# Kernel tuning notes

Hardware: AMD Instinct MI355X
Metric: run time of the kernel (lower is better)

## Reference

```python
import jax, jax.numpy as jnp
import numpy as np

N_RAYS, MAX_S, N_VOX, EMB, HID, L_VIEW = 8192, 64, 100000, 32, 128, 4


def view_pe(d):
    # NeRF positional encoding of view dirs: [N,3] -> [N, 3 + 6*L_VIEW]
    freqs = 2.0 ** jnp.arange(L_VIEW, dtype=d.dtype)
    ang = (d[..., None] * freqs).reshape(*d.shape[:-1], -1)  # [N, 3*L]
    return jnp.concatenate([d, jnp.sin(ang), jnp.cos(ang)], -1)


def setup_inputs() -> dict:
    key = jax.random.key(0)
    ks = jax.random.split(key, 16)
    rays_d = jax.random.normal(ks[0], (N_RAYS, 3), dtype=jnp.float32)
    rays_d = rays_d / jnp.linalg.norm(rays_d, axis=-1, keepdims=True)
    pts = jax.random.uniform(ks[1], (N_RAYS, MAX_S, 3), dtype=jnp.float32)
    t_vals = jnp.sort(jax.random.uniform(ks[2], (N_RAYS, MAX_S), dtype=jnp.float32) * 4.0, axis=-1)
    dists = jnp.concatenate([t_vals[:, 1:] - t_vals[:, :-1], jnp.full((N_RAYS, 1), 0.05, jnp.float32)], -1)
    # ragged per-ray sample counts -> -1 padded p2v_idx (as produced by the voxel point sampler)
    counts = jax.random.randint(ks[3], (N_RAYS,), 1, MAX_S + 1)
    ray_hits = jax.random.bernoulli(ks[4], 0.9, (N_RAYS,))
    valid = (jnp.arange(MAX_S)[None, :] < counts[:, None]) & ray_hits[:, None]
    idx = jax.random.randint(ks[5], (N_RAYS, MAX_S), 0, N_VOX)
    p2v_idx = jnp.where(valid, idx, -1).astype(jnp.int32)

    def lin(k, i, o):
        return jax.random.normal(k, (i, o), dtype=jnp.float32) * np.float32(1.0 / np.sqrt(i))

    return dict(
        rays_d=rays_d, pts=pts, t_vals=t_vals, dists=dists,
        p2v_idx=p2v_idx, ray_hits=ray_hits,
        vox_emb=jax.random.normal(ks[6], (N_VOX, EMB), dtype=jnp.float32) * 0.1,
        Wpts=lin(ks[7], 3, EMB),
        W1=lin(ks[8], EMB, HID), b1=jnp.zeros((HID,), jnp.float32),
        W2=lin(ks[9], HID, HID), b2=jnp.zeros((HID,), jnp.float32),
        Wsig=lin(ks[10], HID, 1), bsig=jnp.zeros((1,), jnp.float32),
        Wfeat=lin(ks[11], HID, HID), bfeat=jnp.zeros((HID,), jnp.float32),
        Wc1=lin(ks[12], HID + 3 + 6 * L_VIEW, 64), bc1=jnp.zeros((64,), jnp.float32),
        Wc2=lin(ks[13], 64, 3), bc2=jnp.zeros((3,), jnp.float32),
    )


def reference(rays_d, pts, t_vals, dists, vox_emb, Wpts, W1, b1, W2, b2,
              Wsig, bsig, Wfeat, bfeat, Wc1, bc1, Wc2, bc2, p2v_idx, ray_hits):
    mask = p2v_idx >= 0                                   # [N,S] valid samples (mask_pts)
    idx = jnp.where(mask, p2v_idx, 0)
    # voxel_embedder: per-point voxel embedding gather + positional lift
    ve = vox_emb[idx] + pts @ Wpts                        # [N,S,EMB]
    h = jax.nn.relu(ve @ W1 + b1)
    h = jax.nn.relu(h @ W2 + b2)                          # [N,S,HID]
    sigma = (h @ Wsig + bsig)[..., 0]                     # [N,S]
    feat = h @ Wfeat + bfeat                              # [N,S,HID]
    vemb = view_pe(rays_d)                                # [N,27]
    vemb = jnp.broadcast_to(vemb[:, None, :], (feat.shape[0], feat.shape[1], vemb.shape[-1]))
    c = jax.nn.relu(jnp.concatenate([feat, vemb], -1) @ Wc1 + bc1)
    rgb_raw = c @ Wc2 + bc2                               # [N,S,3]
    # masked_scatter semantics: invalid slots are 0 before the min_color remap
    rgb = (jnp.where(mask[..., None], rgb_raw, 0.0) + 1.0) * 0.5   # min_color = -1
    free_energy = jnp.where(mask, jax.nn.relu(sigma) * dists, 0.0)  # [N,S]
    # volumetric_rendering(with_dist=True)
    shifted = jnp.concatenate([jnp.zeros_like(free_energy[:, :1]), free_energy[:, :-1]], -1)
    T = jnp.exp(-jnp.cumsum(shifted, -1))
    weights = (1.0 - jnp.exp(-free_energy)) * T           # [N,S]
    comp_rgb = jnp.einsum('ns,nsc->nc', weights, rgb)     # [N,3]
    acc = weights.sum(-1)                                 # [N]
    depth = (weights * t_vals).sum(-1)
    disp = 1.0 / jnp.maximum(1e-10, depth / jnp.maximum(acc, 1e-10))
    # fill_in for missed rays (white_bkgd=False -> fill with 0)
    comp_rgb = jnp.where(ray_hits[:, None], comp_rgb, 0.0)
    disp = jnp.where(ray_hits, disp, 0.0)
    acc = jnp.where(ray_hits, acc, 0.0)
    return comp_rgb, disp, acc
```

## Files before the change

kernel.cpp:

```cpp
#include <hip/hip_runtime.h>
#include <stdint.h>


#define NRAYS 8192
#define MAXS  64
#define EMB   32
#define HID   128
#define NPE   27
#define CH    64
#define NPTS  (NRAYS * MAXS)
#define RCAP  16384

#define WS_WCOMB  0
#define WS_WPE    (WS_WCOMB + HID*CH)
#define WS_BCOMB  (WS_WPE + 32*CH)
#define WS_CCINIT (WS_BCOMB + CH)
#define WS_COUNTS (WS_CCINIT + NRAYS*CH)
#define WS_OFFS   (WS_COUNTS + NRAYS)
#define WS_TOTAL  (WS_OFFS + NRAYS)
#define WS_RCNT   (WS_TOTAL + 1)
#define WS_LIST   (WS_TOTAL + 4)
#define WS_PTOUT  (WS_LIST + NPTS)
#define WS_FRAGS  (WS_PTOUT + 4*NPTS)
#define WS_RLIST  (WS_FRAGS + 56*2*64*4)
#define WS_PTSC   (WS_RLIST + RCAP)

typedef __attribute__((ext_vector_type(8))) short bf16x8;
typedef __attribute__((ext_vector_type(4))) float f32x4;
union FI { int i[4]; int4 v; bf16x8 f; };

#define MFMA16(a, b, c) __builtin_amdgcn_mfma_f32_16x16x32_bf16(a, b, c, 0, 0, 0)

__device__ __forceinline__ f32x4 mfma3(bf16x8 ah, bf16x8 al, bf16x8 bh, bf16x8 bl,
                                       f32x4 c) {
  c = MFMA16(al, bh, c);
  c = MFMA16(ah, bl, c);
  c = MFMA16(ah, bh, c);
  return c;
}

__device__ __forceinline__ f32x4 mfma2(bf16x8 ah, bf16x8 bh, bf16x8 bl, f32x4 c) {
  c = MFMA16(ah, bl, c);
  c = MFMA16(ah, bh, c);
  return c;
}

__device__ __forceinline__ void split8(const float* x, bf16x8& hi, bf16x8& lo) {
  FI H, L;
#pragma unroll
  for (int r = 0; r < 4; ++r) {
    unsigned u0 = __float_as_uint(x[2 * r]);
    unsigned u1 = __float_as_uint(x[2 * r + 1]);
    unsigned h0 = u0 & 0xffff0000u, h1 = u1 & 0xffff0000u;
    unsigned l0 = __float_as_uint(x[2 * r] - __uint_as_float(h0));
    unsigned l1 = __float_as_uint(x[2 * r + 1] - __uint_as_float(h1));
    H.i[r] = (int)((h0 >> 16) | (h1 & 0xffff0000u));
    L.i[r] = (int)((l0 >> 16) | (l1 & 0xffff0000u));
  }
  hi = H.f; lo = L.f;
}

__device__ __forceinline__ unsigned short bf16rne(float v) {
  unsigned u = __float_as_uint(v);
  return (unsigned short)((u + 0x7fffu + ((u >> 16) & 1u)) >> 16);
}

__global__ __launch_bounds__(256) void prep_kernel(
    const float* __restrict__ Wfeat, const float* __restrict__ bfeat,
    const float* __restrict__ Wc1, const float* __restrict__ bc1,
    float* __restrict__ ws) {
  int idx = blockIdx.x * 256 + threadIdx.x;
  if (idx < HID * CH) {
    int m = idx >> 6, j = idx & 63;
    float s = 0.f;
    for (int f = 0; f < HID; ++f) s = fmaf(Wfeat[m * HID + f], Wc1[f * CH + j], s);
    ws[WS_WCOMB + idx] = s;
    return;
  }
  idx -= HID * CH;
  if (idx < 32 * CH) {
    int v = idx >> 6, j = idx & 63;
    ws[WS_WPE + idx] = (v < NPE) ? Wc1[(HID + v) * CH + j] : 0.f;
    return;
  }
  idx -= 32 * CH;
  if (idx < CH) {
    float s = bc1[idx];
    for (int f = 0; f < HID; ++f) s = fmaf(bfeat[f], Wc1[f * CH + idx], s);
    ws[WS_BCOMB + idx] = s;
    return;
  }
  idx -= CH;
  if (idx < 2) ((int*)(ws + WS_TOTAL))[idx] = 0;
}

__global__ __launch_bounds__(256) void prep2_kernel(
    const float* __restrict__ W1, const float* __restrict__ W2,
    float* __restrict__ ws) {
  int t = blockIdx.x * 256 + threadIdx.x;
  if (t >= 56 * 64) return;
  const int fid = t >> 6, lane = t & 63;
  const int n16 = lane & 15, quad = lane >> 4;
  float x[8];
  if (fid < 8) {
    const int n = fid * 16 + n16, k0 = quad * 8;
#pragma unroll
    for (int j = 0; j < 8; ++j) x[j] = W1[(k0 + j) * HID + n];
  } else if (fid < 40) {
    const int f = fid - 8, nt = f >> 2, s = f & 3;
    const int n = nt * 16 + n16, k0 = s * 32 + quad * 8;
#pragma unroll
    for (int j = 0; j < 8; ++j) x[j] = W2[(k0 + j) * HID + n];
  } else {
    const int f = fid - 40, nt = f >> 2, s = f & 3;
    const int n = nt * 16 + n16, k0 = s * 32 + quad * 8;
#pragma unroll
    for (int j = 0; j < 8; ++j) x[j] = ws[WS_WCOMB + (k0 + j) * CH + n];
  }
  FI H, L;
#pragma unroll
  for (int r = 0; r < 4; ++r) {
    unsigned u0 = __float_as_uint(x[2 * r]);
    unsigned u1 = __float_as_uint(x[2 * r + 1]);
    unsigned h0 = u0 & 0xffff0000u, h1 = u1 & 0xffff0000u;
    unsigned l0 = __float_as_uint(x[2 * r] - __uint_as_float(h0));
    unsigned l1 = __float_as_uint(x[2 * r + 1] - __uint_as_float(h1));
    H.i[r] = (int)((h0 >> 16) | (h1 & 0xffff0000u));
    L.i[r] = (int)((l0 >> 16) | (l1 & 0xffff0000u));
  }
  int4* o = (int4*)(ws + WS_FRAGS);
  o[(fid * 2 + 0) * 64 + lane] = H.v;
  o[(fid * 2 + 1) * 64 + lane] = L.v;
}

__global__ __launch_bounds__(256) void count_pe_kernel(
    const float* __restrict__ rays_d, const int* __restrict__ p2v,
    float* __restrict__ ws) {
  const int tid = threadIdx.x;
  const int ray = blockIdx.x * 4 + (tid >> 6);
  const int lane = tid & 63;
  const int v = p2v[ray * MAXS + lane];
  const unsigned long long ball = __ballot(v >= 0);
  if (lane == 0) ((int*)(ws + WS_COUNTS))[ray] = __popcll(ball);

  const float d0 = rays_d[ray * 3 + 0];
  const float d1 = rays_d[ray * 3 + 1];
  const float d2 = rays_d[ray * 3 + 2];
  float vemb[NPE];
  vemb[0] = d0; vemb[1] = d1; vemb[2] = d2;
#pragma unroll
  for (int i = 0; i < 3; ++i) {
    const float di = (i == 0) ? d0 : (i == 1) ? d1 : d2;
#pragma unroll
    for (int l = 0; l < 4; ++l) {
      const float ang = di * (float)(1 << l);
      vemb[3 + i * 4 + l] = __sinf(ang);
      vemb[3 + 12 + i * 4 + l] = __cosf(ang);
    }
  }
  float s = ws[WS_BCOMB + lane];
  const float* wpe = ws + WS_WPE;
#pragma unroll
  for (int vv = 0; vv < NPE; ++vv) s = fmaf(vemb[vv], wpe[vv * CH + lane], s);
  ws[WS_CCINIT + ray * CH + lane] = s;
}

__global__ __launch_bounds__(1024) void scan_kernel(float* __restrict__ ws) {
  const int* counts = (const int*)(ws + WS_COUNTS);
  int* offs = (int*)(ws + WS_OFFS);
  int* totalp = (int*)(ws + WS_TOTAL);
  __shared__ int wsum[16];
  const int tid = threadIdx.x;
  const int lane = tid & 63;
  const int base = tid * 8;
  if (tid == 0) ((int*)(ws + WS_RCNT))[0] = 0;
  int c[8], e[8];
  int run = 0;
#pragma unroll
  for (int i = 0; i < 8; ++i) { c[i] = counts[base + i]; e[i] = run; run += c[i]; }
  int inc = run;
#pragma unroll
  for (int off = 1; off < 64; off <<= 1) {
    int u = __shfl_up(inc, off, 64);
    if (lane >= off) inc += u;
  }
  const int wexcl = inc - run;
  if (lane == 63) wsum[tid >> 6] = inc;
  __syncthreads();
  if (tid < 16) {
    int v = wsum[tid];
    int inc2 = v;
#pragma unroll
    for (int off = 1; off < 16; off <<= 1) {
      int u = __shfl_up(inc2, off, 64);
      if (tid >= off) inc2 += u;
    }
    wsum[tid] = inc2 - v;
    if (tid == 15) totalp[0] = inc2;
  }
  __syncthreads();
  const int wbase = wsum[tid >> 6];
#pragma unroll
  for (int i = 0; i < 8; ++i) offs[base + i] = wbase + wexcl + e[i];
}

__global__ __launch_bounds__(256) void list_kernel(
    const int* __restrict__ p2v, const float* __restrict__ pts,
    float* __restrict__ ws) {
  const int tid = threadIdx.x;
  const int ray = blockIdx.x * 4 + (tid >> 6);
  const int lane = tid & 63;
  const int pidx = ray * MAXS + lane;
  const int gidx = p2v[pidx];
  const bool valid = gidx >= 0;
  const unsigned long long ball = __ballot(valid);
  const int rank = __popcll(ball & ((1ull << lane) - 1ull));
  if (valid) {
    const int off = ((const int*)(ws + WS_OFFS))[ray];
    const int slot = off + rank;
    ((int*)(ws + WS_LIST))[slot] = pidx;
    float4 pc;
    pc.x = pts[pidx * 3 + 0];
    pc.y = pts[pidx * 3 + 1];
    pc.z = pts[pidx * 3 + 2];
    pc.w = __int_as_float(gidx);
    ((float4*)(ws + WS_PTSC))[slot] = pc;
  }
}

__device__ __forceinline__ void ve_frag(const float* __restrict__ vox_emb,
                                        const float* __restrict__ Wpts,
                                        float4 pc, int quad,
                                        bf16x8& hi, bf16x8& lo) {
  float x[8];
  const int gidx = __float_as_int(pc.w);
  const float4* vr = (const float4*)vox_emb + gidx * 8 + quad * 2;
  const float4 va = vr[0], vb = vr[1];
  const float px = pc.x, py = pc.y, pz = pc.z;
  const float4* wp = (const float4*)Wpts;
  const float4 wa0 = wp[quad * 2 + 0], wa1 = wp[quad * 2 + 1];
  const float4 wb0 = wp[8 + quad * 2 + 0], wb1 = wp[8 + quad * 2 + 1];
  const float4 wc0 = wp[16 + quad * 2 + 0], wc1 = wp[16 + quad * 2 + 1];
  x[0] = va.x + fmaf(px, wa0.x, fmaf(py, wb0.x, pz * wc0.x));
  x[1] = va.y + fmaf(px, wa0.y, fmaf(py, wb0.y, pz * wc0.y));
  x[2] = va.z + fmaf(px, wa0.z, fmaf(py, wb0.z, pz * wc0.z));
  x[3] = va.w + fmaf(px, wa0.w, fmaf(py, wb0.w, pz * wc0.w));
  x[4] = vb.x + fmaf(px, wa1.x, fmaf(py, wb1.x, pz * wc1.x));
  x[5] = vb.y + fmaf(px, wa1.y, fmaf(py, wb1.y, pz * wc1.y));
  x[6] = vb.z + fmaf(px, wa1.z, fmaf(py, wb1.z, pz * wc1.z));
  x[7] = vb.w + fmaf(px, wa1.w, fmaf(py, wb1.w, pz * wc1.w));
  split8(x, hi, lo);
}

#define SROW 136

__global__ __launch_bounds__(128, 2) void mlp_mfma(
    const float* __restrict__ vox_emb, const float* __restrict__ Wpts,
    const float* __restrict__ b1, const float* __restrict__ b2,
    const float* __restrict__ Wsig, const float* __restrict__ bsig,
    const float* __restrict__ Wc2, const float* __restrict__ bc2,
    float* __restrict__ ws) {
  __shared__ __align__(16) unsigned short alds[32 * SROW];
  const int tid = threadIdx.x;
  const int wave = tid >> 6, lane = tid & 63;
  const int n16 = lane & 15, quad = lane >> 4;
  const int total = ((const int*)(ws + WS_TOTAL))[0];
  const int base = blockIdx.x * 32 + wave * 16;
  if (base >= total) return;
  const int* list = (const int*)(ws + WS_LIST);
  const int slot0 = min(base + n16, total - 1);
  const int pidx0 = list[slot0];
  const float4 pc0 = ((const float4*)(ws + WS_PTSC))[slot0];
  const int4* fb = (const int4*)(ws + WS_FRAGS);

  int4 B1f[16];
#pragma unroll
  for (int i = 0; i < 16; ++i) B1f[i] = fb[i * 64 + lane];

  bf16x8 a0h, a0l;
  ve_frag(vox_emb, Wpts, pc0, quad, a0h, a0l);

  int4 BL[16];
#pragma unroll
  for (int nt = 0; nt < 8; ++nt) {
    BL[2 * nt]     = fb[((8 + nt * 4) * 2 + 0) * 64 + lane];
    BL[2 * nt + 1] = fb[((8 + nt * 4) * 2 + 1) * 64 + lane];
  }

  f32x4 h[8];
#pragma unroll
  for (int nt = 0; nt < 8; ++nt) {
    const float bb = b1[nt * 16 + n16];
    h[nt] = (f32x4){bb, bb, bb, bb};
  }
#pragma unroll
  for (int nt = 0; nt < 8; ++nt) {
    FI H, L; H.v = B1f[2 * nt]; L.v = B1f[2 * nt + 1];
    h[nt] = mfma3(a0h, a0l, H.f, L.f, h[nt]);
  }
#pragma unroll
  for (int nt = 0; nt < 8; ++nt)
#pragma unroll
    for (int r = 0; r < 4; ++r) {
      const float v = fmaxf(h[nt][r], 0.f);
      const int row = wave * 16 + quad * 4 + r;
      const int gk = ((2 * nt + (n16 >> 3)) ^ (row & 7)) << 3;
      alds[row * SROW + gk + (n16 & 7)] = bf16rne(v);
    }

  f32x4 g[8];
#pragma unroll
  for (int nt = 0; nt < 8; ++nt) {
    const float bb = b2[nt * 16 + n16];
    g[nt] = (f32x4){bb, bb, bb, bb};
  }
  const int rrow0 = (wave * 16 + n16) * SROW;
  const int t7 = n16 & 7;
#pragma unroll
  for (int s = 0; s < 4; ++s) {
    const int gq = ((4 * s + quad) ^ t7) << 3;
    const bf16x8 A0h = *(const bf16x8*)&alds[rrow0 + gq];
#pragma unroll
    for (int nt = 0; nt < 8; ++nt) {
      FI H, L; H.v = BL[2 * nt]; L.v = BL[2 * nt + 1];
      g[nt] = mfma2(A0h, H.f, L.f, g[nt]);
    }
    if (s < 3) {
#pragma unroll
      for (int nt = 0; nt < 8; ++nt) {
        BL[2 * nt]     = fb[((8 + nt * 4 + s + 1) * 2 + 0) * 64 + lane];
        BL[2 * nt + 1] = fb[((8 + nt * 4 + s + 1) * 2 + 1) * 64 + lane];
      }
    }
  }

  int pm[4];
#pragma unroll
  for (int r = 0; r < 4; ++r)
    pm[r] = __shfl(pidx0, quad * 4 + r, 64);
  int4 BC[8];
#pragma unroll
  for (int nt = 0; nt < 4; ++nt) {
    BC[2 * nt]     = fb[((40 + nt * 4) * 2 + 0) * 64 + lane];
    BC[2 * nt + 1] = fb[((40 + nt * 4) * 2 + 1) * 64 + lane];
  }
  f32x4 cacc[4];
#pragma unroll
  for (int nt = 0; nt < 4; ++nt)
#pragma unroll
    for (int r = 0; r < 4; ++r)
      cacc[nt][r] = ws[WS_CCINIT + (pm[r] >> 6) * CH + nt * 16 + n16];

  float sg[4] = {0.f, 0.f, 0.f, 0.f};
#pragma unroll
  for (int nt = 0; nt < 8; ++nt) {
    const float sv = Wsig[nt * 16 + n16];
#pragma unroll
    for (int r = 0; r < 4; ++r) {
      const float v = fmaxf(g[nt][r], 0.f);
      sg[r] = fmaf(v, sv, sg[r]);
      const int row = wave * 16 + quad * 4 + r;
      const int gk = ((2 * nt + (n16 >> 3)) ^ (row & 7)) << 3;
      alds[row * SROW + gk + (n16 & 7)] = bf16rne(v);
    }
  }
#pragma unroll
  for (int mask = 1; mask < 16; mask <<= 1)
#pragma unroll
    for (int r = 0; r < 4; ++r) sg[r] += __shfl_xor(sg[r], mask, 64);

#pragma unroll
  for (int s = 0; s < 4; ++s) {
    const int gq = ((4 * s + quad) ^ t7) << 3;
    const bf16x8 A0h = *(const bf16x8*)&alds[rrow0 + gq];
#pragma unroll
    for (int nt = 0; nt < 4; ++nt) {
      FI H, L; H.v = BC[2 * nt]; L.v = BC[2 * nt + 1];
      cacc[nt] = mfma2(A0h, H.f, L.f, cacc[nt]);
    }
    if (s < 3) {
#pragma unroll
      for (int nt = 0; nt < 4; ++nt) {
        BC[2 * nt]     = fb[((40 + nt * 4 + s + 1) * 2 + 0) * 64 + lane];
        BC[2 * nt + 1] = fb[((40 + nt * 4 + s + 1) * 2 + 1) * 64 + lane];
      }
    }
  }

  float cr[3][4];
#pragma unroll
  for (int c = 0; c < 3; ++c)
#pragma unroll
    for (int r = 0; r < 4; ++r) cr[c][r] = 0.f;
#pragma unroll
  for (int nt = 0; nt < 4; ++nt) {
    const int j = nt * 16 + n16;
    const float w0 = Wc2[j * 3 + 0], w1c = Wc2[j * 3 + 1], w2c = Wc2[j * 3 + 2];
#pragma unroll
    for (int r = 0; r < 4; ++r) {
      const float cv = fmaxf(cacc[nt][r], 0.f);
      cr[0][r] = fmaf(cv, w0, cr[0][r]);
      cr[1][r] = fmaf(cv, w1c, cr[1][r]);
      cr[2][r] = fmaf(cv, w2c, cr[2][r]);
    }
  }
#pragma unroll
  for (int mask = 1; mask < 16; mask <<= 1)
#pragma unroll
    for (int c = 0; c < 3; ++c)
#pragma unroll
      for (int r = 0; r < 4; ++r) cr[c][r] += __shfl_xor(cr[c][r], mask, 64);

  if (n16 == 0) {
    const float bs = bsig[0];
    const float bcr = bc2[0], bcg = bc2[1], bcb = bc2[2];
#pragma unroll
    for (int r = 0; r < 4; ++r) {
      const int m = quad * 4 + r;
      if (base + m < total) {
        const int pid = pm[r];
        const float sig = sg[r] + bs;
        ((float4*)(ws + WS_PTOUT))[pid] =
            make_float4(sig, cr[0][r] + bcr, cr[1][r] + bcg, cr[2][r] + bcb);
        if (fabsf(sig) < 0.006f) {
          const int ri = atomicAdd((int*)(ws + WS_RCNT), 1);
          if (ri < RCAP) ((int*)(ws + WS_RLIST))[ri] = pid;
        }
      }
    }
  }
}

__device__ __forceinline__ float wave_sum(float v) {
#pragma unroll
  for (int off = 32; off > 0; off >>= 1) v += __shfl_down(v, off, 64);
  return v;
}

__global__ __launch_bounds__(256) void repair_kernel(
    const float* __restrict__ pts, const int* __restrict__ p2v,
    const float* __restrict__ vox_emb, const float* __restrict__ Wpts,
    const float* __restrict__ W1, const float* __restrict__ b1,
    const float* __restrict__ W2, const float* __restrict__ b2,
    const float* __restrict__ Wsig, const float* __restrict__ bsig,
    float* __restrict__ ws) {
  __shared__ float h1s[4][HID];
  const int wv = threadIdx.x >> 6, lane = threadIdx.x & 63;
  const int cnt = min(((const int*)(ws + WS_RCNT))[0], RCAP);
  const int nw = gridDim.x * 4;
  for (int i = blockIdx.x * 4 + wv; i < cnt; i += nw) {
    const int pidx = ((const int*)(ws + WS_RLIST))[i];
    const int gidx = p2v[pidx];
    const float px = pts[pidx * 3 + 0];
    const float py = pts[pidx * 3 + 1];
    const float pz = pts[pidx * 3 + 2];
    float ve[EMB];
#pragma unroll
    for (int e = 0; e < EMB; ++e)
      ve[e] = vox_emb[gidx * EMB + e] +
              fmaf(px, Wpts[e], fmaf(py, Wpts[EMB + e], pz * Wpts[2 * EMB + e]));
    float s0 = b1[lane], s1 = b1[lane + 64];
#pragma unroll
    for (int k = 0; k < EMB; ++k) {
      const float x = ve[k];
      s0 = fmaf(x, W1[k * HID + lane], s0);
      s1 = fmaf(x, W1[k * HID + lane + 64], s1);
    }
    h1s[wv][lane] = fmaxf(s0, 0.f);
    h1s[wv][lane + 64] = fmaxf(s1, 0.f);
    float t0 = b2[lane], t1 = b2[lane + 64];
    for (int k = 0; k < HID; ++k) {
      const float x = h1s[wv][k];
      t0 = fmaf(x, W2[k * HID + lane], t0);
      t1 = fmaf(x, W2[k * HID + lane + 64], t1);
    }
    float sp = fmaf(fmaxf(t0, 0.f), Wsig[lane], fmaxf(t1, 0.f) * Wsig[lane + 64]);
    sp = wave_sum(sp);
    if (lane == 0) ws[WS_PTOUT + 4 * pidx + 0] = sp + bsig[0];
  }
}

__device__ __forceinline__ float wave_prefix_excl(float v, int lane) {
  float inc = v;
#pragma unroll
  for (int off = 1; off < 64; off <<= 1) {
    float u = __shfl_up(inc, off, 64);
    if (lane >= off) inc += u;
  }
  return inc - v;
}

__global__ __launch_bounds__(256) void render_kernel(
    const float* __restrict__ t_vals, const float* __restrict__ dists,
    const int* __restrict__ p2v, const float* __restrict__ ws,
    float* __restrict__ out_rgb, float* __restrict__ out_disp,
    float* __restrict__ out_acc) {
  const int tid = threadIdx.x;
  const int ray = blockIdx.x * 4 + (tid >> 6);
  const int lane = tid & 63;
  const int pidx = ray * MAXS + lane;

  const int vidx = p2v[pidx];
  const bool hit = (__shfl(vidx, 0, 64) >= 0);
  if (!hit) {
    if (lane < 3) out_rgb[ray * 3 + lane] = 0.f;
    if (lane == 0) { out_disp[ray] = 0.f; out_acc[ray] = 0.f; }
    return;
  }
  const bool valid = vidx >= 0;

  const float4 pv = ((const float4*)(ws + WS_PTOUT))[pidx];
  const float fe = valid ? fmaxf(pv.x, 0.f) * dists[pidx] : 0.f;
  const float pref = wave_prefix_excl(fe, lane);
  const float T = __expf(-pref);
  const float w = (1.f - __expf(-fe)) * T;
  const float tv = t_vals[pidx];

  const float crgb0 = wave_sum(w * (pv.y + 1.f) * 0.5f);
  const float crgb1 = wave_sum(w * (pv.z + 1.f) * 0.5f);
  const float crgb2 = wave_sum(w * (pv.w + 1.f) * 0.5f);
  const float accs = wave_sum(w);
  const float depth = wave_sum(w * tv);

  if (lane == 0) {
    out_rgb[ray * 3 + 0] = crgb0;
    out_rgb[ray * 3 + 1] = crgb1;
    out_rgb[ray * 3 + 2] = crgb2;
    const float disp = 1.f / fmaxf(1e-10f, depth / fmaxf(accs, 1e-10f));
    out_disp[ray] = disp;
    out_acc[ray] = accs;
  }
}

extern "C" void kernel_launch(void* const* d_in, const int* in_sizes, int n_in,
                              void* d_out, int out_size, void* d_ws, size_t ws_size,
                              hipStream_t stream) {
  const float* rays_d  = (const float*)d_in[0];
  const float* pts     = (const float*)d_in[1];
  const float* t_vals  = (const float*)d_in[2];
  const float* dists   = (const float*)d_in[3];
  const int*   p2v     = (const int*)d_in[4];
  const float* vox_emb = (const float*)d_in[6];
  const float* Wpts    = (const float*)d_in[7];
  const float* W1      = (const float*)d_in[8];
  const float* b1      = (const float*)d_in[9];
  const float* W2      = (const float*)d_in[10];
  const float* b2      = (const float*)d_in[11];
  const float* Wsig    = (const float*)d_in[12];
  const float* bsig    = (const float*)d_in[13];
  const float* Wfeat   = (const float*)d_in[14];
  const float* bfeat   = (const float*)d_in[15];
  const float* Wc1     = (const float*)d_in[16];
  const float* bc1     = (const float*)d_in[17];
  const float* Wc2     = (const float*)d_in[18];
  const float* bc2     = (const float*)d_in[19];

  float* ws = (float*)d_ws;
  float* out = (float*)d_out;
  float* out_rgb = out;
  float* out_disp = out + NRAYS * 3;
  float* out_acc = out + NRAYS * 4;

  hipLaunchKernelGGL(prep_kernel, dim3(41), dim3(256), 0, stream,
                     Wfeat, bfeat, Wc1, bc1, ws);
  hipLaunchKernelGGL(prep2_kernel, dim3(14), dim3(256), 0, stream, W1, W2, ws);
  hipLaunchKernelGGL(count_pe_kernel, dim3(NRAYS / 4), dim3(256), 0, stream,
                     rays_d, p2v, ws);
  hipLaunchKernelGGL(scan_kernel, dim3(1), dim3(1024), 0, stream, ws);
  hipLaunchKernelGGL(list_kernel, dim3(NRAYS / 4), dim3(256), 0, stream,
                     p2v, pts, ws);
  hipLaunchKernelGGL(mlp_mfma, dim3(NPTS / 32), dim3(128), 0, stream,
                     vox_emb, Wpts, b1, b2, Wsig, bsig, Wc2, bc2, ws);
  hipLaunchKernelGGL(repair_kernel, dim3(128), dim3(256), 0, stream,
                     pts, p2v, vox_emb, Wpts, W1, b1, W2, b2, Wsig, bsig, ws);
  hipLaunchKernelGGL(render_kernel, dim3(NRAYS / 4), dim3(256), 0, stream,
                     t_vals, dists, p2v, ws, out_rgb, out_disp, out_acc);
}
```

Baseline: 251.2 us.

## Split MLP output columns across waves so each wave reuses weight fragments over 64 points

The MLP kernel now runs a 256-thread block over 64 points. Each wave owns a slice of the output columns for all 64 rows, instead of each wave owning 16 rows and all columns. Weight fragments are loaded once per wave and reused across four row tiles, which cuts per-wave global weight traffic and register pressure from holding all B fragments. In exchange it adds block-wide __syncthreads for the shared activation tile, plus shared-memory partial sums for sigma and rgb that are combined across waves.

```diff
diff --git a/kernel.cpp b/kernel.cpp
--- a/kernel.cpp
+++ b/kernel.cpp
@@ -254,174 +254,233 @@
 
 #define SROW 136
 
-__global__ __launch_bounds__(128, 2) void mlp_mfma(
+__global__ __launch_bounds__(256, 2) void mlp_mfma(
     const float* __restrict__ vox_emb, const float* __restrict__ Wpts,
     const float* __restrict__ b1, const float* __restrict__ b2,
     const float* __restrict__ Wsig, const float* __restrict__ bsig,
     const float* __restrict__ Wc2, const float* __restrict__ bc2,
     float* __restrict__ ws) {
-  __shared__ __align__(16) unsigned short alds[32 * SROW];
+  __shared__ __align__(16) unsigned short alds[64 * SROW];
+  __shared__ float sgp[4][64];
+  __shared__ __align__(16) float4 rgbp[4][64];
   const int tid = threadIdx.x;
   const int wave = tid >> 6, lane = tid & 63;
   const int n16 = lane & 15, quad = lane >> 4;
   const int total = ((const int*)(ws + WS_TOTAL))[0];
-  const int base = blockIdx.x * 32 + wave * 16;
+  const int base = blockIdx.x * 64;
   if (base >= total) return;
   const int* list = (const int*)(ws + WS_LIST);
-  const int slot0 = min(base + n16, total - 1);
-  const int pidx0 = list[slot0];
-  const float4 pc0 = ((const float4*)(ws + WS_PTSC))[slot0];
+
+  int pidx[4]; float4 pc[4];
+#pragma unroll
+  for (int m = 0; m < 4; ++m) {
+    const int slot = min(base + m * 16 + n16, total - 1);
+    pidx[m] = list[slot];
+    pc[m] = ((const float4*)(ws + WS_PTSC))[slot];
+  }
   const int4* fb = (const int4*)(ws + WS_FRAGS);
-
-  int4 B1f[16];
-#pragma unroll
-  for (int i = 0; i < 16; ++i) B1f[i] = fb[i * 64 + lane];
-
-  bf16x8 a0h, a0l;
-  ve_frag(vox_emb, Wpts, pc0, quad, a0h, a0l);
-
-  int4 BL[16];
-#pragma unroll
-  for (int nt = 0; nt < 8; ++nt) {
-    BL[2 * nt]     = fb[((8 + nt * 4) * 2 + 0) * 64 + lane];
-    BL[2 * nt + 1] = fb[((8 + nt * 4) * 2 + 1) * 64 + lane];
-  }
-
-  f32x4 h[8];
-#pragma unroll
-  for (int nt = 0; nt < 8; ++nt) {
-    const float bb = b1[nt * 16 + n16];
-    h[nt] = (f32x4){bb, bb, bb, bb};
-  }
-#pragma unroll
-  for (int nt = 0; nt < 8; ++nt) {
-    FI H, L; H.v = B1f[2 * nt]; L.v = B1f[2 * nt + 1];
-    h[nt] = mfma3(a0h, a0l, H.f, L.f, h[nt]);
-  }
-#pragma unroll
-  for (int nt = 0; nt < 8; ++nt)
-#pragma unroll
-    for (int r = 0; r < 4; ++r) {
-      const float v = fmaxf(h[nt][r], 0.f);
-      const int row = wave * 16 + quad * 4 + r;
-      const int gk = ((2 * nt + (n16 >> 3)) ^ (row & 7)) << 3;
-      alds[row * SROW + gk + (n16 & 7)] = bf16rne(v);
-    }
-
-  f32x4 g[8];
-#pragma unroll
-  for (int nt = 0; nt < 8; ++nt) {
-    const float bb = b2[nt * 16 + n16];
-    g[nt] = (f32x4){bb, bb, bb, bb};
-  }
-  const int rrow0 = (wave * 16 + n16) * SROW;
+  const int nt0 = 2 * wave, nt1 = nt0 + 1;
+
+  int4 B1[4];
+  B1[0] = fb[(nt0 * 2 + 0) * 64 + lane];
+  B1[1] = fb[(nt0 * 2 + 1) * 64 + lane];
+  B1[2] = fb[(nt1 * 2 + 0) * 64 + lane];
+  B1[3] = fb[(nt1 * 2 + 1) * 64 + lane];
+
+  bf16x8 ah[4], al[4];
+#pragma unroll
+  for (int m = 0; m < 4; ++m) ve_frag(vox_emb, Wpts, pc[m], quad, ah[m], al[m]);
+
+  int4 BL[4];
+  BL[0] = fb[((8 + nt0 * 4) * 2 + 0) * 64 + lane];
+  BL[1] = fb[((8 + nt0 * 4) * 2 + 1) * 64 + lane];
+  BL[2] = fb[((8 + nt1 * 4) * 2 + 0) * 64 + lane];
+  BL[3] = fb[((8 + nt1 * 4) * 2 + 1) * 64 + lane];
+
+  f32x4 h[4][2];
+  {
+    const float ba = b1[nt0 * 16 + n16], bb = b1[nt1 * 16 + n16];
+#pragma unroll
+    for (int m = 0; m < 4; ++m) {
+      h[m][0] = (f32x4){ba, ba, ba, ba};
+      h[m][1] = (f32x4){bb, bb, bb, bb};
+    }
+  }
+  {
+    FI H0, L0, H1, L1v;
+    H0.v = B1[0]; L0.v = B1[1]; H1.v = B1[2]; L1v.v = B1[3];
+#pragma unroll
+    for (int m = 0; m < 4; ++m) {
+      h[m][0] = mfma3(ah[m], al[m], H0.f, L0.f, h[m][0]);
+      h[m][1] = mfma3(ah[m], al[m], H1.f, L1v.f, h[m][1]);
+    }
+  }
+#pragma unroll
+  for (int m = 0; m < 4; ++m)
+#pragma unroll
+    for (int j = 0; j < 2; ++j) {
+      const int nt = nt0 + j;
+#pragma unroll
+      for (int r = 0; r < 4; ++r) {
+        const float v = fmaxf(h[m][j][r], 0.f);
+        const int row = m * 16 + quad * 4 + r;
+        const int gk = ((2 * nt + (n16 >> 3)) ^ (row & 7)) << 3;
+        alds[row * SROW + gk + (n16 & 7)] = bf16rne(v);
+      }
+    }
+  __syncthreads();
+
+  f32x4 g[4][2];
+  {
+    const float ba = b2[nt0 * 16 + n16], bb = b2[nt1 * 16 + n16];
+#pragma unroll
+    for (int m = 0; m < 4; ++m) {
+      g[m][0] = (f32x4){ba, ba, ba, ba};
+      g[m][1] = (f32x4){bb, bb, bb, bb};
+    }
+  }
   const int t7 = n16 & 7;
 #pragma unroll
   for (int s = 0; s < 4; ++s) {
     const int gq = ((4 * s + quad) ^ t7) << 3;
-    const bf16x8 A0h = *(const bf16x8*)&alds[rrow0 + gq];
-#pragma unroll
-    for (int nt = 0; nt < 8; ++nt) {
-      FI H, L; H.v = BL[2 * nt]; L.v = BL[2 * nt + 1];
-      g[nt] = mfma2(A0h, H.f, L.f, g[nt]);
+    FI H0, L0, H1, L1v;
+    H0.v = BL[0]; L0.v = BL[1]; H1.v = BL[2]; L1v.v = BL[3];
+#pragma unroll
+    for (int m = 0; m < 4; ++m) {
+      const bf16x8 A = *(const bf16x8*)&alds[(m * 16 + n16) * SROW + gq];
+      g[m][0] = mfma2(A, H0.f, L0.f, g[m][0]);
+      g[m][1] = mfma2(A, H1.f, L1v.f, g[m][1]);
     }
     if (s < 3) {
-#pragma unroll
-      for (int nt = 0; nt < 8; ++nt) {
-        BL[2 * nt]     = fb[((8 + nt * 4 + s + 1) * 2 + 0) * 64 + lane];
-        BL[2 * nt + 1] = fb[((8 + nt * 4 + s + 1) * 2 + 1) * 64 + lane];
+      BL[0] = fb[((8 + nt0 * 4 + s + 1) * 2 + 0) * 64 + lane];
+      BL[1] = fb[((8 + nt0 * 4 + s + 1) * 2 + 1) * 64 + lane];
+      BL[2] = fb[((8 + nt1 * 4 + s + 1) * 2 + 0) * 64 + lane];
+      BL[3] = fb[((8 + nt1 * 4 + s + 1) * 2 + 1) * 64 + lane];
+    }
+  }
+
+  int4 BC[8];
+#pragma unroll
+  for (int s = 0; s < 4; ++s) {
+    BC[2 * s]     = fb[((40 + wave * 4 + s) * 2 + 0) * 64 + lane];
+    BC[2 * s + 1] = fb[((40 + wave * 4 + s) * 2 + 1) * 64 + lane];
+  }
+  int pm[4][4];
+#pragma unroll
+  for (int m = 0; m < 4; ++m)
+#pragma unroll
+    for (int r = 0; r < 4; ++r)
+      pm[m][r] = __shfl(pidx[m], quad * 4 + r, 64);
+  f32x4 cacc[4];
+#pragma unroll
+  for (int m = 0; m < 4; ++m)
+#pragma unroll
+    for (int r = 0; r < 4; ++r)
+      cacc[m][r] = ws[WS_CCINIT + (pm[m][r] >> 6) * CH + wave * 16 + n16];
+
+  __syncthreads();
+
+  float sgv[4][4];
+#pragma unroll
+  for (int m = 0; m < 4; ++m)
+#pragma unroll
+    for (int r = 0; r < 4; ++r) sgv[m][r] = 0.f;
+  {
+    const float sv0 = Wsig[nt0 * 16 + n16], sv1 = Wsig[nt1 * 16 + n16];
+#pragma unroll
+    for (int m = 0; m < 4; ++m)
+#pragma unroll
+      for (int j = 0; j < 2; ++j) {
+        const int nt = nt0 + j;
+        const float sv = j ? sv1 : sv0;
+#pragma unroll
+        for (int r = 0; r < 4; ++r) {
+          const float v = fmaxf(g[m][j][r], 0.f);
+          sgv[m][r] = fmaf(v, sv, sgv[m][r]);
+          const int row = m * 16 + quad * 4 + r;
+          const int gk = ((2 * nt + (n16 >> 3)) ^ (row & 7)) << 3;
+          alds[row * SROW + gk + (n16 & 7)] = bf16rne(v);
+        }
       }
-    }
-  }
-
-  int pm[4];
-#pragma unroll
-  for (int r = 0; r < 4; ++r)
-    pm[r] = __shfl(pidx0, quad * 4 + r, 64);
-  int4 BC[8];
-#pragma unroll
-  for (int nt = 0; nt < 4; ++nt) {
-    BC[2 * nt]     = fb[((40 + nt * 4) * 2 + 0) * 64 + lane];
-    BC[2 * nt + 1] = fb[((40 + nt * 4) * 2 + 1) * 64 + lane];
-  }
-  f32x4 cacc[4];
-#pragma unroll
-  for (int nt = 0; nt < 4; ++nt)
-#pragma unroll
-    for (int r = 0; r < 4; ++r)
-      cacc[nt][r] = ws[WS_CCINIT + (pm[r] >> 6) * CH + nt * 16 + n16];
-
-  float sg[4] = {0.f, 0.f, 0.f, 0.f};
-#pragma unroll
-  for (int nt = 0; nt < 8; ++nt) {
-    const float sv = Wsig[nt * 16 + n16];
-#pragma unroll
-    for (int r = 0; r < 4; ++r) {
-      const float v = fmaxf(g[nt][r], 0.f);
-      sg[r] = fmaf(v, sv, sg[r]);
-      const int row = wave * 16 + quad * 4 + r;
-      const int gk = ((2 * nt + (n16 >> 3)) ^ (row & 7)) << 3;
-      alds[row * SROW + gk + (n16 & 7)] = bf16rne(v);
-    }
   }
 #pragma unroll
   for (int mask = 1; mask < 16; mask <<= 1)
 #pragma unroll
-    for (int r = 0; r < 4; ++r) sg[r] += __shfl_xor(sg[r], mask, 64);
+    for (int m = 0; m < 4; ++m)
+#pragma unroll
+      for (int r = 0; r < 4; ++r)
+        sgv[m][r] += __shfl_xor(sgv[m][r], mask, 64);
+  if (n16 == 0) {
+#pragma unroll
+    for (int m = 0; m < 4; ++m)
+#pragma unroll
+      for (int r = 0; r < 4; ++r)
+        sgp[wave][m * 16 + quad * 4 + r] = sgv[m][r];
+  }
+  __syncthreads();
 
 #pragma unroll
   for (int s = 0; s < 4; ++s) {
     const int gq = ((4 * s + quad) ^ t7) << 3;
-    const bf16x8 A0h = *(const bf16x8*)&alds[rrow0 + gq];
-#pragma unroll
-    for (int nt = 0; nt < 4; ++nt) {
-      FI H, L; H.v = BC[2 * nt]; L.v = BC[2 * nt + 1];
-      cacc[nt] = mfma2(A0h, H.f, L.f, cacc[nt]);
-    }
-    if (s < 3) {
-#pragma unroll
-      for (int nt = 0; nt < 4; ++nt) {
-        BC[2 * nt]     = fb[((40 + nt * 4 + s + 1) * 2 + 0) * 64 + lane];
-        BC[2 * nt + 1] = fb[((40 + nt * 4 + s + 1) * 2 + 1) * 64 + lane];
+    FI H, L;
+    H.v = BC[2 * s]; L.v = BC[2 * s + 1];
+#pragma unroll
+    for (int m = 0; m < 4; ++m) {
+      const bf16x8 A = *(const bf16x8*)&alds[(m * 16 + n16) * SROW + gq];
+      cacc[m] = mfma2(A, H.f, L.f, cacc[m]);
+    }
+  }
+
+  {
+    const int j = wave * 16 + n16;
+    const float w0 = Wc2[j * 3 + 0], w1c = Wc2[j * 3 + 1], w2c = Wc2[j * 3 + 2];
+#pragma unroll
+    for (int m = 0; m < 4; ++m) {
+      float c0[4], c1[4], c2[4];
+#pragma unroll
+      for (int r = 0; r < 4; ++r) {
+        const float cv = fmaxf(cacc[m][r], 0.f);
+        c0[r] = cv * w0; c1[r] = cv * w1c; c2[r] = cv * w2c;
       }
-    }
-  }
-
-  float cr[3][4];
-#pragma unroll
-  for (int c = 0; c < 3; ++c)
-#pragma unroll
-    for (int r = 0; r < 4; ++r) cr[c][r] = 0.f;
-#pragma unroll
-  for (int nt = 0; nt < 4; ++nt) {
-    const int j = nt * 16 + n16;
-    const float w0 = Wc2[j * 3 + 0], w1c = Wc2[j * 3 + 1], w2c = Wc2[j * 3 + 2];
-#pragma unroll
-    for (int r = 0; r < 4; ++r) {
-      const float cv = fmaxf(cacc[nt][r], 0.f);
-      cr[0][r] = fmaf(cv, w0, cr[0][r]);
-      cr[1][r] = fmaf(cv, w1c, cr[1][r]);
-      cr[2][r] = fmaf(cv, w2c, cr[2][r]);
-    }
-  }
-#pragma unroll
-  for (int mask = 1; mask < 16; mask <<= 1)
-#pragma unroll
-    for (int c = 0; c < 3; ++c)
-#pragma unroll
-      for (int r = 0; r < 4; ++r) cr[c][r] += __shfl_xor(cr[c][r], mask, 64);
+#pragma unroll
+      for (int mask = 1; mask < 16; mask <<= 1)
+#pragma unroll
+        for (int r = 0; r < 4; ++r) {
+          c0[r] += __shfl_xor(c0[r], mask, 64);
+          c1[r] += __shfl_xor(c1[r], mask, 64);
+          c2[r] += __shfl_xor(c2[r], mask, 64);
+        }
+      if (n16 == 0) {
+#pragma unroll
+        for (int r = 0; r < 4; ++r)
+          rgbp[wave][m * 16 + quad * 4 + r] = make_float4(c0[r], c1[r], c2[r], 0.f);
+      }
+    }
+  }
+  __syncthreads();
+
+  const int pidw = (wave == 0) ? pidx[0] : (wave == 1) ? pidx[1]
+                 : (wave == 2) ? pidx[2] : pidx[3];
+  int pmw[4];
+#pragma unroll
+  for (int r = 0; r < 4; ++r) pmw[r] = __shfl(pidw, quad * 4 + r, 64);
 
   if (n16 == 0) {
     const float bs = bsig[0];
     const float bcr = bc2[0], bcg = bc2[1], bcb = bc2[2];
 #pragma unroll
     for (int r = 0; r < 4; ++r) {
-      const int m = quad * 4 + r;
-      if (base + m < total) {
-        const int pid = pm[r];
-        const float sig = sg[r] + bs;
-        ((float4*)(ws + WS_PTOUT))[pid] =
-            make_float4(sig, cr[0][r] + bcr, cr[1][r] + bcg, cr[2][r] + bcb);
+      const int ptl = wave * 16 + quad * 4 + r;
+      if (base + ptl < total) {
+        const int pid = pmw[r];
+        const float sig = sgp[0][ptl] + sgp[1][ptl] + sgp[2][ptl] + sgp[3][ptl] + bs;
+        const float4 r0 = rgbp[0][ptl], r1 = rgbp[1][ptl];
+        const float4 r2 = rgbp[2][ptl], r3 = rgbp[3][ptl];
+        ((float4*)(ws + WS_PTOUT))[pid] = make_float4(
+            sig,
+            r0.x + r1.x + r2.x + r3.x + bcr,
+            r0.y + r1.y + r2.y + r3.y + bcg,
+            r0.z + r1.z + r2.z + r3.z + bcb);
         if (fabsf(sig) < 0.006f) {
           const int ri = atomicAdd((int*)(ws + WS_RCNT), 1);
           if (ri < RCAP) ((int*)(ws + WS_RLIST))[ri] = pid;
@@ -569,7 +628,7 @@
   hipLaunchKernelGGL(scan_kernel, dim3(1), dim3(1024), 0, stream, ws);
   hipLaunchKernelGGL(list_kernel, dim3(NRAYS / 4), dim3(256), 0, stream,
                      p2v, pts, ws);
-  hipLaunchKernelGGL(mlp_mfma, dim3(NPTS / 32), dim3(128), 0, stream,
+  hipLaunchKernelGGL(mlp_mfma, dim3(NPTS / 64), dim3(256), 0, stream,
                      vox_emb, Wpts, b1, b2, Wsig, bsig, Wc2, bc2, ws);
   hipLaunchKernelGGL(repair_kernel, dim3(128), dim3(256), 0, stream,
                      pts, p2v, vox_emb, Wpts, W1, b1, W2, b2, Wsig, bsig, ws);
```

Measured after the change: 248.9 us. Within noise of the previous version (-0.9%).
